# Performance work log

Hardware: AMD Instinct MI355X
Metric: run time of the kernel (lower is better)

The kernel has to match this reference:

```python
import jax, jax.numpy as jnp
import numpy as np

NEG_SLOPE = 0.2

def gat_layer(x, src, dst, W, a_src, a_dst, bias, heads, out_ch, concat):
    N = x.shape[0]
    h = (x @ W).reshape(N, heads, out_ch)                      # [N,H,C]
    alpha_s = jnp.sum(h * a_src, axis=-1)                      # [N,H]
    alpha_d = jnp.sum(h * a_dst, axis=-1)                      # [N,H]
    e = jax.nn.leaky_relu(alpha_s[src] + alpha_d[dst], NEG_SLOPE)  # [E,H]
    m = jax.ops.segment_max(e, dst, num_segments=N)            # segment softmax over incoming edges
    e = jnp.exp(e - m[dst])
    denom = jax.ops.segment_sum(e, dst, num_segments=N)
    alpha = e / denom[dst]                                     # [E,H]
    out = jax.ops.segment_sum(alpha[:, :, None] * h[src], dst, num_segments=N)  # [N,H,C]
    out = out.reshape(N, heads * out_ch) if concat else out.mean(axis=1)
    return out + bias

def _glorot(key, shape, fan):
    return jax.random.normal(key, shape, dtype=jnp.float32) * (1.0 / np.sqrt(fan))

def setup_inputs() -> dict:
    key = jax.random.key(0)
    ks = jax.random.split(key, 16)
    N, E, F_IN, H = 50000, 1600000, 128, 2
    x = jax.random.normal(ks[0], (N, F_IN), dtype=jnp.float32)
    edge_index = jax.random.randint(ks[1], (2, E), 0, N, dtype=jnp.int32)
    w1  = _glorot(ks[2], (F_IN, H * 32), F_IN)
    as1 = _glorot(ks[3], (H, 32), 32); ad1 = _glorot(ks[4], (H, 32), 32)
    b1  = jnp.zeros((H * 32,), jnp.float32)
    w2  = _glorot(ks[5], (H * 32, H * 64), H * 32)
    as2 = _glorot(ks[6], (H, 64), 64); ad2 = _glorot(ks[7], (H, 64), 64)
    b2  = jnp.zeros((H * 64,), jnp.float32)
    # layer 3: 128 -> 64, heads=1, concat=False
    w3  = _glorot(ks[8], (H * 64, 64), H * 64)
    as3 = _glorot(ks[9], (1, 64), 64); ad3 = _glorot(ks[10], (1, 64), 64)
    b3  = jnp.zeros((64,), jnp.float32)
    fcw = _glorot(ks[11], (64, 512), 64)
    fcb = jnp.zeros((512,), jnp.float32)
    return dict(x=x, edge_index=edge_index, w1=w1, as1=as1, ad1=ad1, b1=b1,
                w2=w2, as2=as2, ad2=ad2, b2=b2, w3=w3, as3=as3, ad3=ad3, b3=b3,
                fcw=fcw, fcb=fcb)

def reference(x, edge_index, w1, as1, ad1, b1, w2, as2, ad2, b2, w3, as3, ad3, b3, fcw, fcb):
    N = x.shape[0]
    # PyG GATConv default: add self-loops
    loops = jnp.arange(N, dtype=edge_index.dtype)
    src = jnp.concatenate([edge_index[0], loops])
    dst = jnp.concatenate([edge_index[1], loops])
    h = jax.nn.relu(gat_layer(x, src, dst, w1, as1, ad1, b1, heads=2, out_ch=32, concat=True))
    h = jax.nn.relu(gat_layer(h, src, dst, w2, as2, ad2, b2, heads=2, out_ch=64, concat=True))
    h = jax.nn.relu(gat_layer(h, src, dst, w3, as3, ad3, b3, heads=1, out_ch=64, concat=False))
    return jax.nn.relu(h @ fcw + fcb)
```

## Files before the change

kernel.cpp:

```cpp
#include <hip/hip_runtime.h>
#include <hip/hip_fp16.h>
#include <math.h>


typedef _Float16 h2_t __attribute__((ext_vector_type(2)));
typedef _Float16 f16x8 __attribute__((ext_vector_type(8)));
typedef float f32x4 __attribute__((ext_vector_type(4)));

__device__ __forceinline__ h2_t as_h2(unsigned int u) {
    union { unsigned int u; h2_t h; } x; x.u = u; return x.h;
}

__device__ __forceinline__ float fdot2(h2_t a, h2_t b, float c) {
#if __has_builtin(__builtin_amdgcn_fdot2)
    return __builtin_amdgcn_fdot2(a, b, c, false);
#else
    return c + (float)a[0] * (float)b[0] + (float)a[1] * (float)b[1];
#endif
}

__global__ void cvt_kernel(
        const float* __restrict__ x, __half* __restrict__ xh, int n4,
        const float* __restrict__ w1, const float* __restrict__ w2,
        const float* __restrict__ w3, const float* __restrict__ fcw,
        __half* __restrict__ o1, __half* __restrict__ o2T,
        __half* __restrict__ o3T, __half* __restrict__ o4T,
        int XB) {
    const int b = blockIdx.x;
    if (b < XB) {
        int i = b * 256 + threadIdx.x;
        if (i < n4) {
            float4 v = ((const float4*)x)[i];
            __half2 a, c;
            a.x = (__half)v.x; a.y = (__half)v.y;
            c.x = (__half)v.z; c.y = (__half)v.w;
            ((__half2*)xh)[2 * i]     = a;
            ((__half2*)xh)[2 * i + 1] = c;
        }
    } else {
        int i = (b - XB) * 256 + threadIdx.x;
        if (i < 8192) {
            o1[i] = (__half)w1[i];
        } else if (i < 16384) {
            int j = i - 8192;
            int k = j >> 7, c = j & 127;
            o2T[c * 64 + k] = (__half)w2[j];
        } else if (i < 24576) {
            int j = i - 16384;
            int k = j >> 6, c = j & 63;
            o3T[c * 128 + k] = (__half)w3[j];
        } else if (i < 57344) {
            int j = i - 24576;
            int k = j >> 9, c = j & 511;
            o4T[c * 64 + k] = (__half)fcw[j];
        }
    }
}

#define SCAN_NB 256

__global__ __launch_bounds__(256) void scanA_kernel(const int* __restrict__ cnt,
                                                    int N, int* __restrict__ bsum) {
    __shared__ int red[256];
    const int chunk = (N + SCAN_NB - 1) / SCAN_NB;
    const int lo = blockIdx.x * chunk;
    const int len = min(N - lo, chunk);
    int s = 0;
    for (int i = threadIdx.x; i < len; i += 256) s += cnt[lo + i];
    red[threadIdx.x] = s;
    __syncthreads();
    for (int off = 128; off >= 1; off >>= 1) {
        if (threadIdx.x < off) red[threadIdx.x] += red[threadIdx.x + off];
        __syncthreads();
    }
    if (threadIdx.x == 0) bsum[blockIdx.x] = red[0];
}

__global__ __launch_bounds__(256) void scanB_kernel(int* __restrict__ bsum,
                                                    int* __restrict__ bbase) {
    __shared__ int s[256];
    int v = bsum[threadIdx.x];
    s[threadIdx.x] = v;
    __syncthreads();
    for (int off = 1; off < 256; off <<= 1) {
        int t = (threadIdx.x >= off) ? s[threadIdx.x - off] : 0;
        __syncthreads();
        s[threadIdx.x] += t;
        __syncthreads();
    }
    bbase[threadIdx.x] = s[threadIdx.x] - v;
}

__global__ __launch_bounds__(256) void scanC_kernel(const int* __restrict__ cnt,
                                                    int N, int Etot,
                                                    const int* __restrict__ bbase,
                                                    int* __restrict__ row_ptr) {
    __shared__ int s[256];
    const int chunk = (N + SCAN_NB - 1) / SCAN_NB;
    const int lo = blockIdx.x * chunk;
    const int len = min(N - lo, chunk);
    const int t = threadIdx.x;
    int v = (t < len) ? cnt[lo + t] : 0;
    s[t] = v;
    __syncthreads();
    for (int off = 1; off < 256; off <<= 1) {
        int u = (t >= off) ? s[t - off] : 0;
        __syncthreads();
        s[t] += u;
        __syncthreads();
    }
    if (t < len) row_ptr[lo + t] = bbase[blockIdx.x] + s[t] - v;
    if (blockIdx.x == 0 && t == 0) row_ptr[N] = Etot;
}

__global__ void scatter_kernel(const int* __restrict__ ei, int E, int N,
                               const int* __restrict__ row_ptr,
                               const int* __restrict__ rank,
                               int* __restrict__ csr_src) {
    const int Etot = E + N;
    const int T = gridDim.x * blockDim.x;
    int e = blockIdx.x * blockDim.x + threadIdx.x;
#pragma unroll 4
    for (int u = 0; u < 4; ++u, e += T) {
        if (e < Etot) {
            int src, dst;
            if (e < E) { src = ei[e]; dst = ei[E + e]; }
            else       { src = e - E; dst = e - E; }
            csr_src[row_ptr[dst] + rank[e]] = src;
        }
    }
}

__global__ __launch_bounds__(256) void gemm1_count_kernel(
        const __half* __restrict__ in,
        const __half* __restrict__ Wh,
        __half* __restrict__ out,
        const float* __restrict__ a_src,
        const float* __restrict__ a_dst,
        float* __restrict__ alpS,
        float* __restrict__ alpD,
        int N,
        const int* __restrict__ ei, int E,
        int* __restrict__ cnt, int* __restrict__ rank,
        int GGEMM) {
    constexpr int K4 = 32, CHUNK = 64, M = 64, RB = 8;
    __shared__ uint2 wlds[K4 * CHUNK];

    if (blockIdx.x >= GGEMM) {
        const int Etot = E + N;
        const int T = (gridDim.x - GGEMM) * 256;
        int e = (blockIdx.x - GGEMM) * 256 + threadIdx.x;
#pragma unroll 7
        for (int u = 0; u < 7; ++u, e += T) {
            if (e < Etot) {
                int dst = (e < E) ? ei[E + e] : (e - E);
                rank[e] = atomicAdd(&cnt[dst], 1);
            }
        }
        return;
    }

    const unsigned short* wsrc = (const unsigned short*)Wh;
    for (int idx = threadIdx.x; idx < K4 * CHUNK; idx += 256) {
        int k4 = idx / CHUNK, c = idx % CHUNK;
        const unsigned short* wp = wsrc + (size_t)(4 * k4) * M + c;
        uint2 v;
        v.x = (unsigned int)wp[0]     | ((unsigned int)wp[M] << 16);
        v.y = (unsigned int)wp[2 * M] | ((unsigned int)wp[3 * M] << 16);
        wlds[idx] = v;
    }
    __syncthreads();

    const int wid  = threadIdx.x >> 6;
    const int lane = threadIdx.x & 63;
    const float aSv = a_src[lane];
    const float aDv = a_dst[lane];

    const int groups = (N + RB - 1) / RB;
    for (int g = blockIdx.x * 4 + wid; g < groups; g += GGEMM * 4) {
        const int n0 = g * RB;
        const bool full = (n0 + RB <= N);

        float acc[RB];
#pragma unroll
        for (int r = 0; r < RB; ++r) acc[r] = 0.0f;

        const uint2* xp = (const uint2*)(in + (size_t)n0 * 128);

        if (full) {
            uint2 xv[RB], xn[RB];
#pragma unroll
            for (int r = 0; r < RB; ++r) xv[r] = xp[r * K4];
#pragma unroll 2
            for (int k4 = 0; k4 < K4; ++k4) {
                if (k4 + 1 < K4) {
#pragma unroll
                    for (int r = 0; r < RB; ++r)
                        xn[r] = xp[r * K4 + k4 + 1];
                }
                uint2 wv = wlds[k4 * CHUNK + lane];
#pragma unroll
                for (int r = 0; r < RB; ++r) {
                    acc[r] = fdot2(as_h2(xv[r].x), as_h2(wv.x), acc[r]);
                    acc[r] = fdot2(as_h2(xv[r].y), as_h2(wv.y), acc[r]);
                }
                if (k4 + 1 < K4) {
#pragma unroll
                    for (int r = 0; r < RB; ++r) xv[r] = xn[r];
                }
            }
        } else {
#pragma unroll 1
            for (int k4 = 0; k4 < K4; ++k4) {
                uint2 wv = wlds[k4 * CHUNK + lane];
#pragma unroll 1
                for (int r = 0; r < RB; ++r) {
                    if (n0 + r >= N) break;
                    uint2 xr = xp[(size_t)r * K4 + k4];
                    acc[r] = fdot2(as_h2(xr.x), as_h2(wv.x), acc[r]);
                    acc[r] = fdot2(as_h2(xr.y), as_h2(wv.y), acc[r]);
                }
            }
        }

#pragma unroll
        for (int r = 0; r < RB; ++r) {
            if (!full && n0 + r >= N) break;
            const int n = n0 + r;
            out[(size_t)n * M + lane] = (__half)acc[r];

            float ps = acc[r] * aSv, pd = acc[r] * aDv;
            for (int mm = 16; mm >= 1; mm >>= 1) {
                ps += __shfl_xor(ps, mm, 64);
                pd += __shfl_xor(pd, mm, 64);
            }
            if ((lane & 31) == 0) {
                int idx = n * 2 + (lane >> 5);
                alpS[idx] = ps; alpD[idx] = pd;
            }
        }
    }
}

__global__ __launch_bounds__(256) void gemm2_mfma_kernel(
        const __half* __restrict__ in,
        const __half* __restrict__ WT,
        __half* __restrict__ out,
        const float* __restrict__ a_src,
        const float* __restrict__ a_dst,
        float* __restrict__ alpS,
        float* __restrict__ alpD,
        int N, int NT) {
    const int wid     = threadIdx.x >> 6;
    const int lane    = threadIdx.x & 63;
    const int rowgrp  = wid >> 1;
    const int colhalf = wid & 1;
    const int cb = colhalf * 64;
    const int r  = lane & 15;
    const int kg = lane >> 4;

    f16x8 bfrag[4][2];
#pragma unroll
    for (int t = 0; t < 4; ++t)
#pragma unroll
        for (int kf = 0; kf < 2; ++kf)
            bfrag[t][kf] = *(const f16x8*)(WT + (size_t)(cb + t * 16 + r) * 64 + kf * 32 + kg * 8);
    float asv[4], adv[4];
#pragma unroll
    for (int t = 0; t < 4; ++t) {
        asv[t] = a_src[cb + t * 16 + r];
        adv[t] = a_dst[cb + t * 16 + r];
    }

    const int rt = blockIdx.x * 2 + rowgrp;
    if (rt >= NT) return;
    const int n0 = rt * 16;

    f16x8 a0 = *(const f16x8*)(in + (size_t)(n0 + r) * 64 + kg * 8);
    f16x8 a1 = *(const f16x8*)(in + (size_t)(n0 + r) * 64 + 32 + kg * 8);

    f32x4 acc[4];
#pragma unroll
    for (int t = 0; t < 4; ++t) {
        acc[t] = (f32x4){0.0f, 0.0f, 0.0f, 0.0f};
        acc[t] = __builtin_amdgcn_mfma_f32_16x16x32_f16(a0, bfrag[t][0], acc[t], 0, 0, 0);
        acc[t] = __builtin_amdgcn_mfma_f32_16x16x32_f16(a1, bfrag[t][1], acc[t], 0, 0, 0);
    }

#pragma unroll
    for (int i = 0; i < 4; ++i) {
        int grow = n0 + kg * 4 + i;
        if (grow < N) {
#pragma unroll
            for (int t = 0; t < 4; ++t)
                out[(size_t)grow * 128 + cb + t * 16 + r] = (__half)acc[t][i];
        }
    }
    float ps[4], pd[4];
#pragma unroll
    for (int i = 0; i < 4; ++i) {
        ps[i] = acc[0][i] * asv[0] + acc[1][i] * asv[1] + acc[2][i] * asv[2] + acc[3][i] * asv[3];
        pd[i] = acc[0][i] * adv[0] + acc[1][i] * adv[1] + acc[2][i] * adv[2] + acc[3][i] * adv[3];
    }
    for (int mm = 8; mm >= 1; mm >>= 1) {
#pragma unroll
        for (int i = 0; i < 4; ++i) {
            ps[i] += __shfl_xor(ps[i], mm, 64);
            pd[i] += __shfl_xor(pd[i], mm, 64);
        }
    }
    if (r == 0) {
#pragma unroll
        for (int i = 0; i < 4; ++i) {
            int n = n0 + kg * 4 + i;
            if (n < N) {
                alpS[n * 2 + colhalf] = ps[i];
                alpD[n * 2 + colhalf] = pd[i];
            }
        }
    }
}

__global__ __launch_bounds__(256) void gemm3_mfma_kernel(
        const __half* __restrict__ in,
        const __half* __restrict__ WT,
        __half* __restrict__ out,
        const float* __restrict__ a_src,
        const float* __restrict__ a_dst,
        float* __restrict__ alpS,
        float* __restrict__ alpD,
        int N, int NT) {
    const int wid  = threadIdx.x >> 6;
    const int lane = threadIdx.x & 63;
    const int r  = lane & 15;
    const int kg = lane >> 4;

    f16x8 bfrag[4][4];
#pragma unroll
    for (int t = 0; t < 4; ++t)
#pragma unroll
        for (int kf = 0; kf < 4; ++kf)
            bfrag[t][kf] = *(const f16x8*)(WT + (size_t)(t * 16 + r) * 128 + kf * 32 + kg * 8);
    float asv[4], adv[4];
#pragma unroll
    for (int t = 0; t < 4; ++t) {
        asv[t] = a_src[t * 16 + r];
        adv[t] = a_dst[t * 16 + r];
    }

    const int rt = blockIdx.x * 4 + wid;
    if (rt >= NT) return;
    const int n0 = rt * 16;

    f16x8 a[4];
#pragma unroll
    for (int kf = 0; kf < 4; ++kf)
        a[kf] = *(const f16x8*)(in + (size_t)(n0 + r) * 128 + kf * 32 + kg * 8);

    f32x4 acc[4];
#pragma unroll
    for (int t = 0; t < 4; ++t) {
        acc[t] = (f32x4){0.0f, 0.0f, 0.0f, 0.0f};
#pragma unroll
        for (int kf = 0; kf < 4; ++kf)
            acc[t] = __builtin_amdgcn_mfma_f32_16x16x32_f16(a[kf], bfrag[t][kf], acc[t], 0, 0, 0);
    }

#pragma unroll
    for (int i = 0; i < 4; ++i) {
        int grow = n0 + kg * 4 + i;
        if (grow < N) {
#pragma unroll
            for (int t = 0; t < 4; ++t)
                out[(size_t)grow * 64 + t * 16 + r] = (__half)acc[t][i];
        }
    }
    float ps[4], pd[4];
#pragma unroll
    for (int i = 0; i < 4; ++i) {
        ps[i] = acc[0][i] * asv[0] + acc[1][i] * asv[1] + acc[2][i] * asv[2] + acc[3][i] * asv[3];
        pd[i] = acc[0][i] * adv[0] + acc[1][i] * adv[1] + acc[2][i] * adv[2] + acc[3][i] * adv[3];
    }
    for (int mm = 8; mm >= 1; mm >>= 1) {
#pragma unroll
        for (int i = 0; i < 4; ++i) {
            ps[i] += __shfl_xor(ps[i], mm, 64);
            pd[i] += __shfl_xor(pd[i], mm, 64);
        }
    }
    if (r == 0) {
#pragma unroll
        for (int i = 0; i < 4; ++i) {
            int n = n0 + kg * 4 + i;
            if (n < N) { alpS[n] = ps[i]; alpD[n] = pd[i]; }
        }
    }
}

__global__ __launch_bounds__(256) void fcmfma_kernel(
        const __half* __restrict__ in,
        const __half* __restrict__ WT,
        const float* __restrict__ bias,
        float* __restrict__ out,
        int N, int NT) {
    const int wid  = threadIdx.x >> 6;
    const int lane = threadIdx.x & 63;
    const int cb = blockIdx.y * 256 + wid * 64;
    const int r  = lane & 15;
    const int kg = lane >> 4;

    f16x8 bfrag[4][2];
#pragma unroll
    for (int t = 0; t < 4; ++t)
#pragma unroll
        for (int kf = 0; kf < 2; ++kf)
            bfrag[t][kf] = *(const f16x8*)(WT + (size_t)(cb + t * 16 + r) * 64 + kf * 32 + kg * 8);
    float bs[4];
#pragma unroll
    for (int t = 0; t < 4; ++t) bs[t] = bias[cb + t * 16 + r];

    const int rt0 = blockIdx.x * 5;
#pragma unroll 1
    for (int q = 0; q < 5; ++q) {
        const int rt = rt0 + q;
        if (rt >= NT) break;
        const int n0 = rt * 16;
        f16x8 a0 = *(const f16x8*)(in + (size_t)(n0 + r) * 64 + kg * 8);
        f16x8 a1 = *(const f16x8*)(in + (size_t)(n0 + r) * 64 + 32 + kg * 8);
#pragma unroll
        for (int t = 0; t < 4; ++t) {
            f32x4 acc = {0.0f, 0.0f, 0.0f, 0.0f};
            acc = __builtin_amdgcn_mfma_f32_16x16x32_f16(a0, bfrag[t][0], acc, 0, 0, 0);
            acc = __builtin_amdgcn_mfma_f32_16x16x32_f16(a1, bfrag[t][1], acc, 0, 0, 0);
#pragma unroll
            for (int i = 0; i < 4; ++i) {
                int grow = n0 + kg * 4 + i;
                if (grow < N)
                    out[(size_t)grow * 512 + cb + t * 16 + r] = fmaxf(acc[i] + bs[t], 0.0f);
            }
        }
    }
}

template <int H, int C>
__global__ __launch_bounds__(256) void aggregate_kernel(
        const __half* __restrict__ h,
        const float* __restrict__ alpha_s,
        const float* __restrict__ alpha_d,
        const int* __restrict__ row_ptr,
        const int* __restrict__ csr_src,
        const float* __restrict__ bias,
        __half* __restrict__ out, int N) {
    constexpr int M = H * C;
    __shared__ int   ss[4][64];
    __shared__ float sp[4][128];
    const int wid  = threadIdx.x >> 6;
    const int lane = threadIdx.x & 63;
    const int n = blockIdx.x * 4 + wid;
    if (n >= N) return;

    const int lo = row_ptr[n], hi = row_ptr[n + 1];
    const int myhead = (H == 2) ? (lane / C) : 0;

    float adv[H];
#pragma unroll
    for (int t = 0; t < H; ++t) adv[t] = alpha_d[n * H + t];

    float m[H], den[H], acc = 0.0f;
#pragma unroll
    for (int t = 0; t < H; ++t) { m[t] = -INFINITY; den[t] = 0.0f; }

    for (int e0 = lo; e0 < hi; e0 += 64) {
        const int idx = e0 + lane;
        const bool valid = idx < hi;
        const int src_l = csr_src[valid ? idx : hi - 1];

        float lg[H];
        if (H == 2) {
            float2 as = ((const float2*)alpha_s)[src_l];
            lg[0] = as.x + adv[0];
            lg[1] = as.y + adv[1];
        } else {
            lg[0] = alpha_s[src_l] + adv[0];
        }
#pragma unroll
        for (int t = 0; t < H; ++t) {
            float v = lg[t];
            v = v > 0.0f ? v : 0.2f * v;
            lg[t] = valid ? v : -INFINITY;
        }
        float cm[H];
#pragma unroll
        for (int t = 0; t < H; ++t) cm[t] = lg[t];
        for (int mm = 32; mm >= 1; mm >>= 1) {
#pragma unroll
            for (int t = 0; t < H; ++t)
                cm[t] = fmaxf(cm[t], __shfl_xor(cm[t], mm, 64));
        }
        float sc[H];
#pragma unroll
        for (int t = 0; t < H; ++t) {
            float mnew = fmaxf(m[t], cm[t]);
            sc[t] = __expf(m[t] - mnew);
            den[t] *= sc[t];
            m[t] = mnew;
        }
        acc *= (H == 1) ? sc[0] : (myhead == 0 ? sc[0] : sc[1]);

        float p[H], dsum[H];
#pragma unroll
        for (int t = 0; t < H; ++t) { p[t] = __expf(lg[t] - m[t]); dsum[t] = p[t]; }
        for (int mm = 32; mm >= 1; mm >>= 1) {
#pragma unroll
            for (int t = 0; t < H; ++t)
                dsum[t] += __shfl_xor(dsum[t], mm, 64);
        }
#pragma unroll
        for (int t = 0; t < H; ++t) den[t] += dsum[t];

        ss[wid][lane] = src_l;
        if (H == 2) ((float2*)sp[wid])[lane] = make_float2(p[0], p[1]);
        else        sp[wid][lane] = p[0];

        int nu = hi - e0; if (nu > 64) nu = 64;
        int u = 0;
#pragma unroll 1
        for (; u + 8 <= nu; u += 8) {
            int su[8];
#pragma unroll
            for (int t = 0; t < 8; ++t)
                su[t] = __builtin_amdgcn_readfirstlane(ss[wid][u + t]);
            float hv[8];
#pragma unroll
            for (int t = 0; t < 8; ++t)
                hv[t] = __half2float(h[(size_t)su[t] * M + lane]);
            if (H == 2) {
                const float2* pb = (const float2*)sp[wid];
#pragma unroll
                for (int t = 0; t < 8; ++t) {
                    float2 q = pb[u + t];
                    acc += (myhead == 0 ? q.x : q.y) * hv[t];
                }
            } else {
#pragma unroll
                for (int t = 0; t < 8; ++t)
                    acc += sp[wid][u + t] * hv[t];
            }
        }
#pragma unroll 1
        for (; u < nu; ++u) {
            int su = __builtin_amdgcn_readfirstlane(ss[wid][u]);
            float hv = __half2float(h[(size_t)su * M + lane]);
            if (H == 2) {
                float2 q = ((const float2*)sp[wid])[u];
                acc += (myhead == 0 ? q.x : q.y) * hv;
            } else {
                acc += sp[wid][u] * hv;
            }
        }
    }

    float dv = (H == 1) ? den[0] : (myhead == 0 ? den[0] : den[1]);
    float v = acc / dv + bias[lane];
    out[(size_t)n * M + lane] = (__half)fmaxf(v, 0.0f);
}

__global__ __launch_bounds__(256) void aggregate2_kernel(
        const __half* __restrict__ h,
        const float* __restrict__ alpha_s,
        const float* __restrict__ alpha_d,
        const int* __restrict__ row_ptr,
        const int* __restrict__ csr_src,
        const float* __restrict__ bias,
        __half* __restrict__ out, int N) {
    __shared__ int   ss[4][64];
    __shared__ float sp[4][64];
    const int wid  = threadIdx.x >> 6;
    const int lane = threadIdx.x & 63;
    const int gw   = blockIdx.x * 4 + wid;
    const int n    = gw >> 1;
    const int hd   = gw & 1;
    if (n >= N) return;

    const int lo = row_ptr[n], hi = row_ptr[n + 1];
    const float adv = alpha_d[n * 2 + hd];

    float m = -INFINITY, den = 0.0f, acc = 0.0f;

    for (int e0 = lo; e0 < hi; e0 += 64) {
        const int idx = e0 + lane;
        const bool valid = idx < hi;
        const int src_l = csr_src[valid ? idx : hi - 1];

        float lg = alpha_s[src_l * 2 + hd] + adv;
        lg = lg > 0.0f ? lg : 0.2f * lg;
        if (!valid) lg = -INFINITY;

        float cm = lg;
        for (int mm = 32; mm >= 1; mm >>= 1)
            cm = fmaxf(cm, __shfl_xor(cm, mm, 64));

        float mnew = fmaxf(m, cm);
        float sc = __expf(m - mnew);
        den *= sc; acc *= sc; m = mnew;

        float p = __expf(lg - m), ds = p;
        for (int mm = 32; mm >= 1; mm >>= 1)
            ds += __shfl_xor(ds, mm, 64);
        den += ds;

        ss[wid][lane] = src_l;
        sp[wid][lane] = p;

        int nu = hi - e0; if (nu > 64) nu = 64;
        int u = 0;
#pragma unroll 1
        for (; u + 8 <= nu; u += 8) {
            int su[8];
#pragma unroll
            for (int t = 0; t < 8; ++t)
                su[t] = __builtin_amdgcn_readfirstlane(ss[wid][u + t]);
            float hv[8];
#pragma unroll
            for (int t = 0; t < 8; ++t)
                hv[t] = __half2float(h[(size_t)su[t] * 128 + hd * 64 + lane]);
#pragma unroll
            for (int t = 0; t < 8; ++t)
                acc += sp[wid][u + t] * hv[t];
        }
#pragma unroll 1
        for (; u < nu; ++u) {
            int su = __builtin_amdgcn_readfirstlane(ss[wid][u]);
            acc += sp[wid][u] * __half2float(h[(size_t)su * 128 + hd * 64 + lane]);
        }
    }

    float v = acc / den + bias[hd * 64 + lane];
    out[(size_t)n * 128 + hd * 64 + lane] = (__half)fmaxf(v, 0.0f);
}


extern "C" void kernel_launch(void* const* d_in, const int* in_sizes, int n_in,
                              void* d_out, int out_size, void* d_ws, size_t ws_size,
                              hipStream_t stream) {
    const float* x   = (const float*)d_in[0];
    const int*   ei  = (const int*)  d_in[1];
    const float* w1  = (const float*)d_in[2];
    const float* as1 = (const float*)d_in[3];
    const float* ad1 = (const float*)d_in[4];
    const float* b1  = (const float*)d_in[5];
    const float* w2  = (const float*)d_in[6];
    const float* as2 = (const float*)d_in[7];
    const float* ad2 = (const float*)d_in[8];
    const float* b2  = (const float*)d_in[9];
    const float* w3  = (const float*)d_in[10];
    const float* as3 = (const float*)d_in[11];
    const float* ad3 = (const float*)d_in[12];
    const float* b3  = (const float*)d_in[13];
    const float* fcw = (const float*)d_in[14];
    const float* fcb = (const float*)d_in[15];
    float* out = (float*)d_out;

    const int N = in_sizes[0] / 128;
    const int E = in_sizes[1] / 2;
    const int Etot = E + N;

    char* p = (char*)d_ws;
    auto alloc = [&](size_t bytes) {
        char* r = p;
        p += (bytes + 255) & ~(size_t)255;
        return r;
    };
    int*    cnt     = (int*)   alloc((size_t)N * 4);
    int*    row_ptr = (int*)   alloc((size_t)(N + 1) * 4);
    int*    rank    = (int*)   alloc((size_t)Etot * 4);
    int*    csr_src = (int*)   alloc((size_t)Etot * 4);
    int*    bsum    = (int*)   alloc((size_t)SCAN_NB * 4);
    int*    bbase   = (int*)   alloc((size_t)SCAN_NB * 4);
    __half* x16     = (__half*)alloc((size_t)N * 128 * 2);
    __half* bufA    = (__half*)alloc((size_t)(N + 16) * 128 * 2);
    __half* bufB    = (__half*)alloc((size_t)(N + 16) * 128 * 2);
    __half* bufC    = (__half*)alloc((size_t)(N + 16) * 64 * 2);
    __half* wh1     = (__half*)alloc((size_t)8192 * 2);
    __half* wh2T    = (__half*)alloc((size_t)8192 * 2);
    __half* wh3T    = (__half*)alloc((size_t)8192 * 2);
    __half* fcwT    = (__half*)alloc((size_t)32768 * 2);
    float*  alpS    = (float*) alloc((size_t)N * 2 * 4);
    float*  alpD    = (float*) alloc((size_t)N * 2 * 4);
    (void)ws_size; (void)n_in; (void)out_size;

    hipMemsetAsync(cnt, 0, (size_t)N * 4, stream);
    const int n4 = N * 32;
    const int XB = (n4 + 255) / 256;
    const int WB = 224;
    cvt_kernel<<<XB + WB, 256, 0, stream>>>(
        x, x16, n4, w1, w2, w3, fcw, wh1, wh2T, wh3T, fcwT, XB);

    int gb  = (N + 3) / 4;
    int gb2 = (2 * N + 3) / 4;
    const int GG1 = 1024;
    const int GC1 = 1024;
    const int NT  = (N + 15) / 16;

    gemm1_count_kernel<<<dim3(GG1 + GC1, 1), 256, 0, stream>>>(
        x16, wh1, bufA, as1, ad1, alpS, alpD, N, ei, E, cnt, rank, GG1);

    scanA_kernel<<<SCAN_NB, 256, 0, stream>>>(cnt, N, bsum);
    scanB_kernel<<<1, 256, 0, stream>>>(bsum, bbase);
    scanC_kernel<<<SCAN_NB, 256, 0, stream>>>(cnt, N, Etot, bbase, row_ptr);
    const int CB = (Etot / 4 + 255) / 256 + 1;
    scatter_kernel<<<CB, 256, 0, stream>>>(ei, E, N, row_ptr, rank, csr_src);

    aggregate_kernel<2, 32><<<gb, 256, 0, stream>>>(bufA, alpS, alpD, row_ptr, csr_src, b1, bufB, N);

    gemm2_mfma_kernel<<<(NT + 1) / 2, 256, 0, stream>>>(
        bufB, wh2T, bufA, as2, ad2, alpS, alpD, N, NT);
    aggregate2_kernel<<<gb2, 256, 0, stream>>>(bufA, alpS, alpD, row_ptr, csr_src, b2, bufB, N);

    gemm3_mfma_kernel<<<(NT + 3) / 4, 256, 0, stream>>>(
        bufB, wh3T, bufA, as3, ad3, alpS, alpD, N, NT);
    aggregate_kernel<1, 64><<<gb, 256, 0, stream>>>(bufA, alpS, alpD, row_ptr, csr_src, b3, bufC, N);

    const int GX = (NT + 4) / 5;
    fcmfma_kernel<<<dim3(GX, 2), 256, 0, stream>>>(
        bufC, fcwT, fcb, out, N, NT);
}
```

Baseline: 517.8 us.

## Split 64-wide features into 32-channel slabs and aggregate each slab separately

The GEMM1 and GEMM3 outputs are now written as two column slabs of 32 channels each, so every node row in a slab is 64 bytes. The aggregation kernel for layers 1 and 3 loops over the two slabs. Within a slab, the two half-waves each gather a different set of edges and are then combined with a shuffle. The aim is to gather smaller contiguous rows per edge and improve cache locality per pass. The cost is recomputing the softmax logits for every slab, which for the single-head layer 3 repeats the whole softmax twice. Reads from LDS also replace the readfirstlane broadcast.

```diff
diff --git a/kernel.cpp b/kernel.cpp
--- a/kernel.cpp
+++ b/kernel.cpp
@@ -139,11 +139,11 @@
         const float* __restrict__ a_dst,
         float* __restrict__ alpS,
         float* __restrict__ alpD,
-        int N,
+        int N, size_t slabstride,
         const int* __restrict__ ei, int E,
         int* __restrict__ cnt, int* __restrict__ rank,
         int GGEMM) {
-    constexpr int K4 = 32, CHUNK = 64, M = 64, RB = 8;
+    constexpr int K4 = 32, CHUNK = 64, RB = 8;
     __shared__ uint2 wlds[K4 * CHUNK];
 
     if (blockIdx.x >= GGEMM) {
@@ -163,10 +163,10 @@
     const unsigned short* wsrc = (const unsigned short*)Wh;
     for (int idx = threadIdx.x; idx < K4 * CHUNK; idx += 256) {
         int k4 = idx / CHUNK, c = idx % CHUNK;
-        const unsigned short* wp = wsrc + (size_t)(4 * k4) * M + c;
+        const unsigned short* wp = wsrc + (size_t)(4 * k4) * 64 + c;
         uint2 v;
-        v.x = (unsigned int)wp[0]     | ((unsigned int)wp[M] << 16);
-        v.y = (unsigned int)wp[2 * M] | ((unsigned int)wp[3 * M] << 16);
+        v.x = (unsigned int)wp[0]   | ((unsigned int)wp[64] << 16);
+        v.y = (unsigned int)wp[128] | ((unsigned int)wp[192] << 16);
         wlds[idx] = v;
     }
     __syncthreads();
@@ -175,6 +175,8 @@
     const int lane = threadIdx.x & 63;
     const float aSv = a_src[lane];
     const float aDv = a_dst[lane];
+    const size_t sbase = (size_t)(lane >> 5) * slabstride;
+    const int ch = lane & 31;
 
     const int groups = (N + RB - 1) / RB;
     for (int g = blockIdx.x * 4 + wid; g < groups; g += GGEMM * 4) {
@@ -227,7 +229,7 @@
         for (int r = 0; r < RB; ++r) {
             if (!full && n0 + r >= N) break;
             const int n = n0 + r;
-            out[(size_t)n * M + lane] = (__half)acc[r];
+            out[sbase + (size_t)n * 32 + ch] = (__half)acc[r];
 
             float ps = acc[r] * aSv, pd = acc[r] * aDv;
             for (int mm = 16; mm >= 1; mm >>= 1) {
@@ -329,7 +331,7 @@
         const float* __restrict__ a_dst,
         float* __restrict__ alpS,
         float* __restrict__ alpD,
-        int N, int NT) {
+        int N, int NT, size_t slabstride) {
     const int wid  = threadIdx.x >> 6;
     const int lane = threadIdx.x & 63;
     const int r  = lane & 15;
@@ -371,8 +373,10 @@
         int grow = n0 + kg * 4 + i;
         if (grow < N) {
 #pragma unroll
-            for (int t = 0; t < 4; ++t)
-                out[(size_t)grow * 64 + t * 16 + r] = (__half)acc[t][i];
+            for (int t = 0; t < 4; ++t) {
+                int col = t * 16 + r;
+                out[(size_t)(col >> 5) * slabstride + (size_t)grow * 32 + (col & 31)] = (__half)acc[t][i];
+            }
         }
     }
     float ps[4], pd[4];
@@ -442,127 +446,79 @@
     }
 }
 
-template <int H, int C>
-__global__ __launch_bounds__(256) void aggregate_kernel(
+template <int H>
+__global__ __launch_bounds__(256) void aggregate_slab_kernel(
         const __half* __restrict__ h,
         const float* __restrict__ alpha_s,
         const float* __restrict__ alpha_d,
         const int* __restrict__ row_ptr,
         const int* __restrict__ csr_src,
         const float* __restrict__ bias,
-        __half* __restrict__ out, int N) {
-    constexpr int M = H * C;
+        __half* __restrict__ out,
+        int N, size_t slabstride) {
     __shared__ int   ss[4][64];
-    __shared__ float sp[4][128];
+    __shared__ float sp[4][64];
     const int wid  = threadIdx.x >> 6;
     const int lane = threadIdx.x & 63;
     const int n = blockIdx.x * 4 + wid;
     if (n >= N) return;
 
     const int lo = row_ptr[n], hi = row_ptr[n + 1];
-    const int myhead = (H == 2) ? (lane / C) : 0;
-
-    float adv[H];
-#pragma unroll
-    for (int t = 0; t < H; ++t) adv[t] = alpha_d[n * H + t];
-
-    float m[H], den[H], acc = 0.0f;
-#pragma unroll
-    for (int t = 0; t < H; ++t) { m[t] = -INFINITY; den[t] = 0.0f; }
-
-    for (int e0 = lo; e0 < hi; e0 += 64) {
-        const int idx = e0 + lane;
-        const bool valid = idx < hi;
-        const int src_l = csr_src[valid ? idx : hi - 1];
-
-        float lg[H];
-        if (H == 2) {
-            float2 as = ((const float2*)alpha_s)[src_l];
-            lg[0] = as.x + adv[0];
-            lg[1] = as.y + adv[1];
-        } else {
-            lg[0] = alpha_s[src_l] + adv[0];
-        }
-#pragma unroll
-        for (int t = 0; t < H; ++t) {
-            float v = lg[t];
-            v = v > 0.0f ? v : 0.2f * v;
-            lg[t] = valid ? v : -INFINITY;
-        }
-        float cm[H];
-#pragma unroll
-        for (int t = 0; t < H; ++t) cm[t] = lg[t];
-        for (int mm = 32; mm >= 1; mm >>= 1) {
-#pragma unroll
-            for (int t = 0; t < H; ++t)
-                cm[t] = fmaxf(cm[t], __shfl_xor(cm[t], mm, 64));
-        }
-        float sc[H];
-#pragma unroll
-        for (int t = 0; t < H; ++t) {
-            float mnew = fmaxf(m[t], cm[t]);
-            sc[t] = __expf(m[t] - mnew);
-            den[t] *= sc[t];
-            m[t] = mnew;
-        }
-        acc *= (H == 1) ? sc[0] : (myhead == 0 ? sc[0] : sc[1]);
-
-        float p[H], dsum[H];
-#pragma unroll
-        for (int t = 0; t < H; ++t) { p[t] = __expf(lg[t] - m[t]); dsum[t] = p[t]; }
-        for (int mm = 32; mm >= 1; mm >>= 1) {
-#pragma unroll
-            for (int t = 0; t < H; ++t)
-                dsum[t] += __shfl_xor(dsum[t], mm, 64);
-        }
-#pragma unroll
-        for (int t = 0; t < H; ++t) den[t] += dsum[t];
-
-        ss[wid][lane] = src_l;
-        if (H == 2) ((float2*)sp[wid])[lane] = make_float2(p[0], p[1]);
-        else        sp[wid][lane] = p[0];
-
-        int nu = hi - e0; if (nu > 64) nu = 64;
-        int u = 0;
+    const int ch = lane & 31;
+    const int eh = lane >> 5;
+
 #pragma unroll 1
-        for (; u + 8 <= nu; u += 8) {
-            int su[8];
-#pragma unroll
-            for (int t = 0; t < 8; ++t)
-                su[t] = __builtin_amdgcn_readfirstlane(ss[wid][u + t]);
-            float hv[8];
-#pragma unroll
-            for (int t = 0; t < 8; ++t)
-                hv[t] = __half2float(h[(size_t)su[t] * M + lane]);
-            if (H == 2) {
-                const float2* pb = (const float2*)sp[wid];
+    for (int slab = 0; slab < 2; ++slab) {
+        const __half* hs = h + (size_t)slab * slabstride;
+        const float adv = (H == 2) ? alpha_d[n * 2 + slab] : alpha_d[n];
+
+        float m = -INFINITY, den = 0.0f, acc = 0.0f;
+
+        for (int e0 = lo; e0 < hi; e0 += 64) {
+            const int idx = e0 + lane;
+            const bool valid = idx < hi;
+            const int src_l = csr_src[valid ? idx : hi - 1];
+
+            float lg = ((H == 2) ? alpha_s[src_l * 2 + slab] : alpha_s[src_l]) + adv;
+            lg = lg > 0.0f ? lg : 0.2f * lg;
+            if (!valid) lg = -INFINITY;
+
+            float cm = lg;
+            for (int mm = 32; mm >= 1; mm >>= 1)
+                cm = fmaxf(cm, __shfl_xor(cm, mm, 64));
+
+            float mnew = fmaxf(m, cm);
+            float sc = __expf(m - mnew);
+            den *= sc; acc *= sc; m = mnew;
+
+            float p = __expf(lg - m), ds = p;
+            for (int mm = 32; mm >= 1; mm >>= 1)
+                ds += __shfl_xor(ds, mm, 64);
+            den += ds;
+
+            ss[wid][lane] = src_l;
+            sp[wid][lane] = p;
+
+            const int nu = min(hi - e0, 64);
+#pragma unroll 1
+            for (int u = 0; u < nu; u += 16) {
 #pragma unroll
                 for (int t = 0; t < 8; ++t) {
-                    float2 q = pb[u + t];
-                    acc += (myhead == 0 ? q.x : q.y) * hv[t];
+                    int eidx = u + eh * 8 + t;
+                    if (eidx < nu) {
+                        int su = ss[wid][eidx];
+                        acc += sp[wid][eidx] * __half2float(hs[(size_t)su * 32 + ch]);
+                    }
                 }
-            } else {
-#pragma unroll
-                for (int t = 0; t < 8; ++t)
-                    acc += sp[wid][u + t] * hv[t];
-            }
-        }
-#pragma unroll 1
-        for (; u < nu; ++u) {
-            int su = __builtin_amdgcn_readfirstlane(ss[wid][u]);
-            float hv = __half2float(h[(size_t)su * M + lane]);
-            if (H == 2) {
-                float2 q = ((const float2*)sp[wid])[u];
-                acc += (myhead == 0 ? q.x : q.y) * hv;
-            } else {
-                acc += sp[wid][u] * hv;
-            }
-        }
-    }
-
-    float dv = (H == 1) ? den[0] : (myhead == 0 ? den[0] : den[1]);
-    float v = acc / dv + bias[lane];
-    out[(size_t)n * M + lane] = (__half)fmaxf(v, 0.0f);
+            }
+        }
+
+        acc += __shfl_xor(acc, 32, 64);
+        if (eh == 0) {
+            float v = acc / den + bias[slab * 32 + ch];
+            out[(size_t)n * 64 + slab * 32 + ch] = (__half)fmaxf(v, 0.0f);
+        }
+    }
 }
 
 __global__ __launch_bounds__(256) void aggregate2_kernel(
@@ -664,6 +620,7 @@
     const int N = in_sizes[0] / 128;
     const int E = in_sizes[1] / 2;
     const int Etot = E + N;
+    const size_t slabstride = (size_t)(N + 16) * 32;
 
     char* p = (char*)d_ws;
     auto alloc = [&](size_t bytes) {
@@ -703,7 +660,7 @@
     const int NT  = (N + 15) / 16;
 
     gemm1_count_kernel<<<dim3(GG1 + GC1, 1), 256, 0, stream>>>(
-        x16, wh1, bufA, as1, ad1, alpS, alpD, N, ei, E, cnt, rank, GG1);
+        x16, wh1, bufA, as1, ad1, alpS, alpD, N, slabstride, ei, E, cnt, rank, GG1);
 
     scanA_kernel<<<SCAN_NB, 256, 0, stream>>>(cnt, N, bsum);
     scanB_kernel<<<1, 256, 0, stream>>>(bsum, bbase);
@@ -711,15 +668,17 @@
     const int CB = (Etot / 4 + 255) / 256 + 1;
     scatter_kernel<<<CB, 256, 0, stream>>>(ei, E, N, row_ptr, rank, csr_src);
 
-    aggregate_kernel<2, 32><<<gb, 256, 0, stream>>>(bufA, alpS, alpD, row_ptr, csr_src, b1, bufB, N);
+    aggregate_slab_kernel<2><<<gb, 256, 0, stream>>>(
+        bufA, alpS, alpD, row_ptr, csr_src, b1, bufB, N, slabstride);
 
     gemm2_mfma_kernel<<<(NT + 1) / 2, 256, 0, stream>>>(
         bufB, wh2T, bufA, as2, ad2, alpS, alpD, N, NT);
     aggregate2_kernel<<<gb2, 256, 0, stream>>>(bufA, alpS, alpD, row_ptr, csr_src, b2, bufB, N);
 
     gemm3_mfma_kernel<<<(NT + 3) / 4, 256, 0, stream>>>(
-        bufB, wh3T, bufA, as3, ad3, alpS, alpD, N, NT);
-    aggregate_kernel<1, 64><<<gb, 256, 0, stream>>>(bufA, alpS, alpD, row_ptr, csr_src, b3, bufC, N);
+        bufB, wh3T, bufA, as3, ad3, alpS, alpD, N, NT, slabstride);
+    aggregate_slab_kernel<1><<<gb, 256, 0, stream>>>(
+        bufA, alpS, alpD, row_ptr, csr_src, b3, bufC, N, slabstride);
 
     const int GX = (NT + 4) / 5;
     fcmfma_kernel<<<dim3(GX, 2), 256, 0, stream>>>(
```

Result: slower. 669.6 us (+29.3%).
